# Kernel tuning notes

Measured on AMD Instinct MI355X. Metric: run time of the kernel, lower is better.

## Reference

```python
import jax, jax.numpy as jnp
import numpy as np

# Static config (init_kwargs)
H = 56; W = 56; C = 256; NH = 8; WS = 7; SS = 3
HD = C // NH
SCALE = HD ** -0.5
N = WS * WS                      # tokens per window = 49
NW = (H // WS) * (W // WS)       # windows per image = 64
HIDDEN = int(C * 4.0)
EPS = 1e-5


def _rel_pos_index():
    coords = np.stack(np.meshgrid(np.arange(WS), np.arange(WS), indexing='ij')).reshape(2, -1)
    rel = coords[:, :, None] - coords[:, None, :]          # [2, N, N]
    rel = rel.transpose(1, 2, 0).astype(np.int64)          # [N, N, 2]
    rel[:, :, 0] += WS - 1
    rel[:, :, 1] += WS - 1
    rel[:, :, 0] *= 2 * WS - 1
    return rel.sum(-1).reshape(-1)                         # [N*N]


def _attn_mask():
    # (0 / -100) mask for the shifted-window configuration, [NW, N, N]
    img = np.zeros([H, W])
    cnt = 0
    for hs in (slice(0, -WS), slice(-WS, -SS), slice(-SS, None)):
        for ws in (slice(0, -WS), slice(-WS, -SS), slice(-SS, None)):
            img[hs, ws] = cnt
            cnt += 1
    mw = img.reshape(H // WS, WS, W // WS, WS).transpose(0, 2, 1, 3).reshape(-1, N)
    diff = mw[:, None, :] - mw[:, :, None]                 # [NW, N, N]
    return np.where(diff != 0, -100.0, 0.0).astype(np.float32)


_REL_IDX = _rel_pos_index()
_MASK = _attn_mask()


def _ln(x, g, b):
    mu = jnp.mean(x, axis=-1, keepdims=True)
    var = jnp.mean((x - mu) ** 2, axis=-1, keepdims=True)
    return (x - mu) * jax.lax.rsqrt(var + EPS) * g + b


def setup_inputs() -> dict:
    key = jax.random.key(0)
    ks = jax.random.split(key, 16)
    B = 32
    s = 0.02
    return {
        'x': jax.random.normal(ks[0], (B, H * W, C), dtype=jnp.float32),
        'gamma1': jnp.ones((C,), jnp.float32),
        'beta1': jnp.zeros((C,), jnp.float32),
        'qkv_w': jax.random.normal(ks[1], (C, 3 * C), jnp.float32) * s,
        'qkv_b': jnp.zeros((3 * C,), jnp.float32),
        'proj_w': jax.random.normal(ks[2], (C, C), jnp.float32) * s,
        'proj_b': jnp.zeros((C,), jnp.float32),
        'rpb_table': jax.random.normal(ks[3], ((2 * WS - 1) * (2 * WS - 1), NH), jnp.float32) * s,
        'gamma2': jnp.ones((C,), jnp.float32),
        'beta2': jnp.zeros((C,), jnp.float32),
        'fc1_w': jax.random.normal(ks[4], (C, HIDDEN), jnp.float32) * s,
        'fc1_b': jnp.zeros((HIDDEN,), jnp.float32),
        'fc2_w': jax.random.normal(ks[5], (HIDDEN, C), jnp.float32) * s,
        'fc2_b': jnp.zeros((C,), jnp.float32),
    }


def reference(x, gamma1, beta1, qkv_w, qkv_b, proj_w, proj_b, rpb_table,
              gamma2, beta2, fc1_w, fc1_b, fc2_w, fc2_b):
    B = x.shape[0]
    y = _ln(x, gamma1, beta1).reshape(B, H, W, C)
    # cyclic shift
    y = jnp.roll(y, (-SS, -SS), axis=(1, 2))
    # window partition -> [B*NW, N, C]
    win = y.reshape(B, H // WS, WS, W // WS, WS, C)
    win = win.transpose(0, 1, 3, 2, 4, 5).reshape(-1, N, C)
    # qkv projection, split heads
    qkv = (win @ qkv_w + qkv_b).reshape(-1, N, 3, NH, HD).transpose(2, 0, 3, 1, 4)
    q, k, v = qkv[0] * SCALE, qkv[1], qkv[2]            # [B*NW, NH, N, HD]
    attn = jnp.einsum('bhnd,bhmd->bhnm', q, k)          # [B*NW, NH, N, N]
    # gathered relative position bias
    bias = rpb_table[jnp.asarray(_REL_IDX)].reshape(N, N, NH).transpose(2, 0, 1)
    attn = attn + bias[None]
    # shift mask
    mask = jnp.asarray(_MASK)                           # [NW, N, N]
    attn = attn.reshape(B, NW, NH, N, N) + mask[None, :, None]
    attn = jax.nn.softmax(attn.reshape(-1, NH, N, N), axis=-1)
    o = jnp.einsum('bhnm,bhmd->bnhd', attn, v).reshape(-1, N, C)
    o = o @ proj_w + proj_b
    # window reverse + reverse shift
    o = o.reshape(B, H // WS, W // WS, WS, WS, C).transpose(0, 1, 3, 2, 4, 5).reshape(B, H, W, C)
    o = jnp.roll(o, (SS, SS), axis=(1, 2)).reshape(B, H * W, C)
    x = x + o
    # MLP block
    y = _ln(x, gamma2, beta2)
    y = jax.nn.gelu(y @ fc1_w + fc1_b, approximate=False) @ fc2_w + fc2_b
    return x + y
```

## Files before the change

### kernel.cpp

```cpp
#include <hip/hip_runtime.h>
#include <hip/hip_bf16.h>
#include <math.h>


typedef __bf16 bf16_t;
typedef __bf16 bf16x4 __attribute__((ext_vector_type(4)));
typedef __bf16 bf16x8 __attribute__((ext_vector_type(8)));
typedef float f32x4 __attribute__((ext_vector_type(4)));

#define AS1 __attribute__((address_space(1)))
#define AS3 __attribute__((address_space(3)))

__device__ __forceinline__ void gload_lds16(const bf16_t* g, bf16_t* l) {
  __builtin_amdgcn_global_load_lds((AS1 void*)g, (AS3 void*)l, 16, 0, 0);
}

__global__ void transpose_cast(const float* __restrict__ w, bf16_t* __restrict__ wt,
                               int K, int N) {
  int idx = blockIdx.x * 256 + threadIdx.x;
  if (idx < N * K) {
    int n = idx / K, k = idx - n * K;
    wt[idx] = (bf16_t)w[(size_t)k * N + n];
  }
}

__global__ void build_bm(const float* __restrict__ rpb, float* __restrict__ bm) {
  int t = blockIdx.x, h = blockIdx.y;
  int wr = (t & 2) ? 7 : 0, wc = (t & 1) ? 7 : 0;
  for (int e = threadIdx.x; e < 4096; e += 256) {
    int r = e >> 6, c = e & 63;
    float v;
    if (c >= 49) {
      v = -30000.f;
    } else if (r >= 49) {
      v = 0.f;
    } else {
      int r1 = r / 7, c1 = r - r1 * 7;
      int r2 = c / 7, c2 = c - r2 * 7;
      v = rpb[((r1 - r2 + 6) * 13 + (c1 - c2 + 6)) * 8 + h];
      int hp = wr * 7 + r1, wp = wc * 7 + c1;
      int hq = wr * 7 + r2, wq = wc * 7 + c2;
      int ri = (hp < 49 ? 0 : (hp < 53 ? 1 : 2)) * 3 + (wp < 49 ? 0 : (wp < 53 ? 1 : 2));
      int rj = (hq < 49 ? 0 : (hq < 53 ? 1 : 2)) * 3 + (wq < 49 ? 0 : (wq < 53 ? 1 : 2));
      if (ri != rj) v -= 100.f;
    }
    bm[((size_t)(t * 8 + h) * 64 + r) * 64 + c] = v;
  }
}

__global__ __launch_bounds__(256)
void ln_cast(const float* __restrict__ src, const float* __restrict__ gamma,
             const float* __restrict__ beta, bf16_t* __restrict__ dst, int windowed) {
  int row = blockIdx.x * 4 + (threadIdx.x >> 6);
  int lane = threadIdx.x & 63;
  size_t srow;
  if (windowed) {
    int w = row / 49, t = row - w * 49;
    int img = w >> 6, wi = w & 63;
    int wr = wi >> 3, wc = wi & 7;
    int rr = t / 7, cc = t - rr * 7;
    int h = wr * 7 + rr + 3; if (h >= 56) h -= 56;
    int ww = wc * 7 + cc + 3; if (ww >= 56) ww -= 56;
    srow = (size_t)img * 3136 + h * 56 + ww;
  } else {
    srow = row;
  }
  float4 v = *(const float4*)(src + srow * 256 + lane * 4);
  float s = v.x + v.y + v.z + v.w;
  float s2 = v.x * v.x + v.y * v.y + v.z * v.z + v.w * v.w;
#pragma unroll
  for (int off = 32; off > 0; off >>= 1) {
    s += __shfl_xor(s, off);
    s2 += __shfl_xor(s2, off);
  }
  float mu = s * (1.0f / 256.0f);
  float rs = rsqrtf(s2 * (1.0f / 256.0f) - mu * mu + 1e-5f);
  float4 g = *(const float4*)(gamma + lane * 4);
  float4 b = *(const float4*)(beta + lane * 4);
  bf16x4 o;
  o[0] = (bf16_t)((v.x - mu) * rs * g.x + b.x);
  o[1] = (bf16_t)((v.y - mu) * rs * g.y + b.y);
  o[2] = (bf16_t)((v.z - mu) * rs * g.z + b.z);
  o[3] = (bf16_t)((v.w - mu) * rs * g.w + b.w);
  *(bf16x4*)(dst + (size_t)row * 256 + lane * 4) = o;
}

template <int MODE>
__global__ __launch_bounds__(256)
void gemm_bt(const bf16_t* __restrict__ A, const bf16_t* __restrict__ Bt,
             const float* __restrict__ bias,
             bf16_t* Cbf, float* Cf, const float* Res,
             int M, int N, int K) {
  __shared__ __align__(16) bf16_t As[128 * 32];
  __shared__ __align__(16) bf16_t Bs[128 * 32];
  const int tid = threadIdx.x;
  const int lane = tid & 63;
  const int wave = tid >> 6;
  const int wm = wave & 1, wn = wave >> 1;
  const int m0 = blockIdx.x * 128;
  const int n0 = blockIdx.y * 128;

  f32x4 acc[4][4];
#pragma unroll
  for (int i = 0; i < 4; i++)
#pragma unroll
    for (int j = 0; j < 4; j++) acc[i][j] = f32x4{0.f, 0.f, 0.f, 0.f};

  const bf16_t* Ag = A + (size_t)m0 * K;
  const bf16_t* Bg = Bt + (size_t)n0 * K;
  const int lr = lane & 15;
  const int kq = (lane >> 4) * 8;

  for (int k0 = 0; k0 < K; k0 += 32) {
#pragma unroll
    for (int it = 0; it < 2; it++) {
      int slot = it * 256 + tid;
      int row = slot >> 2;
      int ko = (slot & 3) << 3;
      bf16_t* ldsA = As + (it * 256 + wave * 64) * 8;
      bf16_t* ldsB = Bs + (it * 256 + wave * 64) * 8;
      gload_lds16(Ag + (size_t)row * K + k0 + ko, ldsA);
      gload_lds16(Bg + (size_t)row * K + k0 + ko, ldsB);
    }
    __syncthreads();
    bf16x8 af[4], bfr[4];
#pragma unroll
    for (int i = 0; i < 4; i++) {
      af[i]  = *(const bf16x8*)(As + (wm * 64 + i * 16 + lr) * 32 + kq);
      bfr[i] = *(const bf16x8*)(Bs + (wn * 64 + i * 16 + lr) * 32 + kq);
    }
#pragma unroll
    for (int i = 0; i < 4; i++)
#pragma unroll
      for (int j = 0; j < 4; j++)
        acc[i][j] = __builtin_amdgcn_mfma_f32_16x16x32_bf16(af[i], bfr[j], acc[i][j], 0, 0, 0);
    __syncthreads();
  }

  const int quad = lane >> 4;
#pragma unroll
  for (int i = 0; i < 4; i++) {
    int rbase = m0 + wm * 64 + i * 16 + quad * 4;
#pragma unroll
    for (int j = 0; j < 4; j++) {
      int col = n0 + wn * 64 + j * 16 + lr;
      float bi = bias[col];
#pragma unroll
      for (int r = 0; r < 4; r++) {
        int row = rbase + r;
        float v = acc[i][j][r] + bi;
        if (MODE == 1) v = 0.5f * v * (1.0f + erff(v * 0.70710678118654752f));
        if (MODE <= 1) {
          Cbf[(size_t)row * N + col] = (bf16_t)v;
        } else if (MODE == 2) {
          size_t idx = (size_t)row * N + col;
          Cf[idx] = v + Res[idx];
        } else {
          int w = row / 49, t = row - w * 49;
          int img = w >> 6, wi = w & 63;
          int wr = wi >> 3, wc = wi & 7;
          int rr = t / 7, cc = t - rr * 7;
          int h = wr * 7 + rr + 3; if (h >= 56) h -= 56;
          int ww2 = wc * 7 + cc + 3; if (ww2 >= 56) ww2 -= 56;
          size_t idx = ((size_t)img * 3136 + h * 56 + ww2) * 256 + col;
          Cf[idx] = v + Res[idx];
        }
      }
    }
  }
}

__global__ __launch_bounds__(256)
void attn_mfma(const bf16_t* __restrict__ qkv, const float* __restrict__ bm,
               bf16_t* __restrict__ o) {
  __shared__ __align__(16) bf16_t Ps[64 * 72];
  __shared__ __align__(16) bf16_t Vt[32 * 72];
  const int w = blockIdx.x, h = blockIdx.y;
  const int tid = threadIdx.x;
  const int lane = tid & 63, wv = tid >> 6;
  const int lr = lane & 15, quad = lane >> 4;
  const int wi = w & 63;
  const int mtype = (((wi >> 3) == 7) ? 2 : 0) | (((wi & 7) == 7) ? 1 : 0);
  const bf16_t* base = qkv + (size_t)w * 49 * 768 + h * 32;

  for (int e = tid; e < 2048; e += 256) {
    int tok = e >> 5, d = e & 31;
    bf16_t val = (bf16_t)0.f;
    if (tok < 49) val = base[(size_t)tok * 768 + 512 + d];
    Vt[d * 72 + tok] = val;
  }
  __syncthreads();

  bf16x8 zero8;
#pragma unroll
  for (int z = 0; z < 8; z++) zero8[z] = (bf16_t)0.f;

  const int mrow = 16 * wv + lr;
  bf16x8 aq = zero8;
  if (mrow < 49) aq = *(const bf16x8*)(base + (size_t)mrow * 768 + quad * 8);
  f32x4 s[4];
#pragma unroll
  for (int j = 0; j < 4; j++) {
    int nrow = 16 * j + lr;
    bf16x8 bk = zero8;
    if (nrow < 49) bk = *(const bf16x8*)(base + (size_t)nrow * 768 + 256 + quad * 8);
    s[j] = __builtin_amdgcn_mfma_f32_16x16x32_bf16(aq, bk, f32x4{0.f, 0.f, 0.f, 0.f}, 0, 0, 0);
  }

  const float* bmb = bm + ((size_t)(mtype * 8 + h) * 64 + 16 * wv) * 64;
  float inv[4];
#pragma unroll
  for (int reg = 0; reg < 4; reg++) {
    int rl = quad * 4 + reg;
    float v0[4];
    float mx = -1e30f;
#pragma unroll
    for (int j = 0; j < 4; j++) {
      float v = s[j][reg] * 0.17677669529663689f + bmb[rl * 64 + 16 * j + lr];
      v0[j] = v;
      mx = fmaxf(mx, v);
    }
#pragma unroll
    for (int off = 8; off > 0; off >>= 1) mx = fmaxf(mx, __shfl_xor(mx, off));
    float sum = 0.f;
#pragma unroll
    for (int j = 0; j < 4; j++) {
      float e = __expf(v0[j] - mx);
      v0[j] = e;
      sum += e;
    }
#pragma unroll
    for (int off = 8; off > 0; off >>= 1) sum += __shfl_xor(sum, off);
    inv[reg] = 1.0f / sum;
#pragma unroll
    for (int j = 0; j < 4; j++)
      Ps[(16 * wv + rl) * 72 + 16 * j + lr] = (bf16_t)v0[j];
  }

  f32x4 oacc[2];
  oacc[0] = f32x4{0.f, 0.f, 0.f, 0.f};
  oacc[1] = f32x4{0.f, 0.f, 0.f, 0.f};
#pragma unroll
  for (int kk = 0; kk < 2; kk++) {
    bf16x8 ap = *(const bf16x8*)(Ps + (16 * wv + lr) * 72 + kk * 32 + quad * 8);
#pragma unroll
    for (int n = 0; n < 2; n++) {
      bf16x8 bv = *(const bf16x8*)(Vt + (16 * n + lr) * 72 + kk * 32 + quad * 8);
      oacc[n] = __builtin_amdgcn_mfma_f32_16x16x32_bf16(ap, bv, oacc[n], 0, 0, 0);
    }
  }
#pragma unroll
  for (int n = 0; n < 2; n++) {
#pragma unroll
    for (int reg = 0; reg < 4; reg++) {
      int row = 16 * wv + quad * 4 + reg;
      if (row < 49) {
        int d = 16 * n + lr;
        o[((size_t)w * 49 + row) * 256 + h * 32 + d] = (bf16_t)(oacc[n][reg] * inv[reg]);
      }
    }
  }
}

extern "C" void kernel_launch(void* const* d_in, const int* in_sizes, int n_in,
                              void* d_out, int out_size, void* d_ws, size_t ws_size,
                              hipStream_t stream) {
  const float* x      = (const float*)d_in[0];
  const float* g1     = (const float*)d_in[1];
  const float* b1     = (const float*)d_in[2];
  const float* qkv_w  = (const float*)d_in[3];
  const float* qkv_b  = (const float*)d_in[4];
  const float* proj_w = (const float*)d_in[5];
  const float* proj_b = (const float*)d_in[6];
  const float* rpb    = (const float*)d_in[7];
  const float* g2     = (const float*)d_in[8];
  const float* b2     = (const float*)d_in[9];
  const float* fc1_w  = (const float*)d_in[10];
  const float* fc1_b  = (const float*)d_in[11];
  const float* fc2_w  = (const float*)d_in[12];
  const float* fc2_b  = (const float*)d_in[13];
  float* out = (float*)d_out;
  char* ws = (char*)d_ws;

  bf16_t* xw   = (bf16_t*)ws;
  bf16_t* qkv  = (bf16_t*)(ws + 51380224);
  bf16_t* ow   = (bf16_t*)(ws + 205520896);
  bf16_t* hbuf = (bf16_t*)(ws + 51380224);
  bf16_t* y2   = xw;
  bf16_t* qkvWt  = (bf16_t*)(ws + 256901120);
  bf16_t* projWt = qkvWt + 768 * 256;
  bf16_t* fc1Wt  = projWt + 256 * 256;
  bf16_t* fc2Wt  = fc1Wt + 1024 * 256;
  float*  bm     = (float*)fc2Wt;

  transpose_cast<<<(768 * 256 + 255) / 256, 256, 0, stream>>>(qkv_w, qkvWt, 256, 768);
  transpose_cast<<<(256 * 256 + 255) / 256, 256, 0, stream>>>(proj_w, projWt, 256, 256);
  transpose_cast<<<(1024 * 256 + 255) / 256, 256, 0, stream>>>(fc1_w, fc1Wt, 256, 1024);
  build_bm<<<dim3(4, 8), 256, 0, stream>>>(rpb, bm);

  ln_cast<<<25088, 256, 0, stream>>>(x, g1, b1, xw, 1);
  gemm_bt<0><<<dim3(784, 6), 256, 0, stream>>>(xw, qkvWt, qkv_b, qkv, nullptr, nullptr,
                                               100352, 768, 256);
  attn_mfma<<<dim3(2048, 8), 256, 0, stream>>>(qkv, bm, ow);
  transpose_cast<<<(256 * 1024 + 255) / 256, 256, 0, stream>>>(fc2_w, fc2Wt, 1024, 256);
  gemm_bt<3><<<dim3(784, 2), 256, 0, stream>>>(ow, projWt, proj_b, nullptr, out, x,
                                               100352, 256, 256);
  ln_cast<<<25088, 256, 0, stream>>>(out, g2, b2, y2, 0);
  gemm_bt<1><<<dim3(784, 8), 256, 0, stream>>>(y2, fc1Wt, fc1_b, hbuf, nullptr, nullptr,
                                               100352, 1024, 256);
  gemm_bt<2><<<dim3(784, 2), 256, 0, stream>>>(hbuf, fc2Wt, fc2_b, nullptr, out, out,
                                               100352, 256, 1024);
}
```

Measured before the change: 870.1 us.

## Fuse MLP fc1, GELU and fc2 into one kernel keeping hidden activations on-chip

Replaces the separate fc1 (with GELU) and fc2 GEMMs with a single fused_mlp kernel. Each block processes 64 token rows, computes the 1024-wide hidden layer in 128-column chunks into LDS, and accumulates the fc2 output in registers, which removes the large bf16 hidden-buffer write and re-read through HBM. GELU switches from exact erf to a tanh-style approximation built on exp, which adds a small numerical deviation from the reference. Other changes merge three weight transpose launches into one and vectorize the V load in the attention kernel. The fused kernel re-streams all MLP weights from cache for every block with no double buffering and many barriers, which may cost throughput.

```diff
diff --git a/kernel.cpp b/kernel.cpp
--- a/kernel.cpp
+++ b/kernel.cpp
@@ -13,6 +13,25 @@
 
 __device__ __forceinline__ void gload_lds16(const bf16_t* g, bf16_t* l) {
   __builtin_amdgcn_global_load_lds((AS1 void*)g, (AS3 void*)l, 16, 0, 0);
+}
+
+__global__ void transpose_cast3(const float* __restrict__ qkv_w,
+                                const float* __restrict__ proj_w,
+                                const float* __restrict__ fc1_w,
+                                bf16_t* __restrict__ qkvWt,
+                                bf16_t* __restrict__ projWt,
+                                bf16_t* __restrict__ fc1Wt) {
+  int idx = blockIdx.x * 256 + threadIdx.x;
+  const float* w;
+  bf16_t* wt;
+  int N;
+  if (blockIdx.y == 0) { w = qkv_w; wt = qkvWt; N = 768; }
+  else if (blockIdx.y == 1) { w = proj_w; wt = projWt; N = 256; }
+  else { w = fc1_w; wt = fc1Wt; N = 1024; }
+  if (idx < N * 256) {
+    int n = idx >> 8, k = idx & 255;
+    wt[idx] = (bf16_t)w[(size_t)k * N + n];
+  }
 }
 
 __global__ void transpose_cast(const float* __restrict__ w, bf16_t* __restrict__ wt,
@@ -149,12 +168,8 @@
       for (int r = 0; r < 4; r++) {
         int row = rbase + r;
         float v = acc[i][j][r] + bi;
-        if (MODE == 1) v = 0.5f * v * (1.0f + erff(v * 0.70710678118654752f));
-        if (MODE <= 1) {
+        if (MODE == 0) {
           Cbf[(size_t)row * N + col] = (bf16_t)v;
-        } else if (MODE == 2) {
-          size_t idx = (size_t)row * N + col;
-          Cf[idx] = v + Res[idx];
         } else {
           int w = row / 49, t = row - w * 49;
           int img = w >> 6, wi = w & 63;
@@ -183,17 +198,18 @@
   const int mtype = (((wi >> 3) == 7) ? 2 : 0) | (((wi & 7) == 7) ? 1 : 0);
   const bf16_t* base = qkv + (size_t)w * 49 * 768 + h * 32;
 
-  for (int e = tid; e < 2048; e += 256) {
-    int tok = e >> 5, d = e & 31;
-    bf16_t val = (bf16_t)0.f;
-    if (tok < 49) val = base[(size_t)tok * 768 + 512 + d];
-    Vt[d * 72 + tok] = val;
+  bf16x8 zero8;
+#pragma unroll
+  for (int z = 0; z < 8; z++) zero8[z] = (bf16_t)0.f;
+
+  {
+    int tok = tid >> 2, d8 = (tid & 3) * 8;
+    bf16x8 v8 = zero8;
+    if (tok < 49) v8 = *(const bf16x8*)(base + (size_t)tok * 768 + 512 + d8);
+#pragma unroll
+    for (int z = 0; z < 8; z++) Vt[(d8 + z) * 72 + tok] = v8[z];
   }
   __syncthreads();
-
-  bf16x8 zero8;
-#pragma unroll
-  for (int z = 0; z < 8; z++) zero8[z] = (bf16_t)0.f;
 
   const int mrow = 16 * wv + lr;
   bf16x8 aq = zero8;
@@ -257,6 +273,124 @@
       if (row < 49) {
         int d = 16 * n + lr;
         o[((size_t)w * 49 + row) * 256 + h * 32 + d] = (bf16_t)(oacc[n][reg] * inv[reg]);
+      }
+    }
+  }
+}
+
+__global__ __launch_bounds__(256, 2)
+void fused_mlp(const bf16_t* __restrict__ y2, const bf16_t* __restrict__ W1t,
+               const float* __restrict__ b1, const bf16_t* __restrict__ W2t,
+               const float* __restrict__ b2, float* __restrict__ out) {
+  __shared__ __align__(16) bf16_t Ls[64 * 264];
+  __shared__ __align__(16) bf16_t Ws[8192];
+  __shared__ __align__(16) bf16_t Hs[64 * 168];
+  const int tid = threadIdx.x;
+  const int lane = tid & 63, wave = tid >> 6;
+  const int lr = lane & 15, quad = lane >> 4;
+  const int wr = wave & 1, wc = wave >> 1;
+  const int m0 = blockIdx.x * 64;
+
+#pragma unroll
+  for (int it = 0; it < 8; it++) {
+    int slot = it * 256 + tid;
+    int row = slot >> 5, g = slot & 31;
+    bf16x8 v = *(const bf16x8*)(y2 + (size_t)(m0 + row) * 256 + g * 8);
+    *(bf16x8*)(Ls + row * 264 + g * 8) = v;
+  }
+  __syncthreads();
+
+  f32x4 acc2[2][8];
+#pragma unroll
+  for (int i = 0; i < 2; i++)
+#pragma unroll
+    for (int n = 0; n < 8; n++) acc2[i][n] = f32x4{0.f, 0.f, 0.f, 0.f};
+
+  for (int hc = 0; hc < 8; hc++) {
+    f32x4 acc1[2][4];
+#pragma unroll
+    for (int i = 0; i < 2; i++)
+#pragma unroll
+      for (int j = 0; j < 4; j++) acc1[i][j] = f32x4{0.f, 0.f, 0.f, 0.f};
+
+    for (int ks = 0; ks < 4; ks++) {
+      __syncthreads();
+#pragma unroll
+      for (int r = 0; r < 4; r++) {
+        int sub = r >> 1, half = r & 1;
+        int row = half * 64 + (tid >> 2), k8 = tid & 3;
+        const bf16_t* src = W1t + (size_t)(hc * 128 + row) * 256 + ks * 64 + sub * 32 + k8 * 8;
+        gload_lds16(src, Ws + sub * 4096 + half * 2048 + wave * 512);
+      }
+      __syncthreads();
+#pragma unroll
+      for (int kk = 0; kk < 2; kk++) {
+        bf16x8 a[2], b[4];
+#pragma unroll
+        for (int i = 0; i < 2; i++)
+          a[i] = *(const bf16x8*)(Ls + (32 * wr + 16 * i + lr) * 264 + ks * 64 + kk * 32 + quad * 8);
+#pragma unroll
+        for (int j = 0; j < 4; j++)
+          b[j] = *(const bf16x8*)(Ws + kk * 4096 + (64 * wc + 16 * j + lr) * 32 + quad * 8);
+#pragma unroll
+        for (int i = 0; i < 2; i++)
+#pragma unroll
+          for (int j = 0; j < 4; j++)
+            acc1[i][j] = __builtin_amdgcn_mfma_f32_16x16x32_bf16(a[i], b[j], acc1[i][j], 0, 0, 0);
+      }
+    }
+#pragma unroll
+    for (int i = 0; i < 2; i++) {
+#pragma unroll
+      for (int j = 0; j < 4; j++) {
+        float bias1 = b1[hc * 128 + 64 * wc + 16 * j + lr];
+        int hoff = (2 * wc + (j >> 1)) * 40 + (j & 1) * 16 + lr;
+#pragma unroll
+        for (int reg = 0; reg < 4; reg++) {
+          int row_l = 32 * wr + 16 * i + quad * 4 + reg;
+          float v = acc1[i][j][reg] + bias1;
+          float arg = fminf(v * (0.7978845608f + 0.0356774081f * v * v), 15.f);
+          float e = __expf(2.f * arg);
+          float g = v * (e / (e + 1.f));
+          Hs[row_l * 168 + hoff] = (bf16_t)g;
+        }
+      }
+    }
+    for (int ks2 = 0; ks2 < 4; ks2++) {
+      __syncthreads();
+#pragma unroll
+      for (int r = 0; r < 4; r++) {
+        int row = r * 64 + (tid >> 2), k8 = tid & 3;
+        const bf16_t* src = W2t + (size_t)row * 1024 + hc * 128 + ks2 * 32 + k8 * 8;
+        gload_lds16(src, Ws + r * 2048 + wave * 512);
+      }
+      __syncthreads();
+      bf16x8 ah[2], bw[8];
+#pragma unroll
+      for (int i = 0; i < 2; i++)
+        ah[i] = *(const bf16x8*)(Hs + (32 * wr + 16 * i + lr) * 168 + ks2 * 40 + quad * 8);
+#pragma unroll
+      for (int n = 0; n < 8; n++)
+        bw[n] = *(const bf16x8*)(Ws + (128 * wc + 16 * n + lr) * 32 + quad * 8);
+#pragma unroll
+      for (int i = 0; i < 2; i++)
+#pragma unroll
+        for (int n = 0; n < 8; n++)
+          acc2[i][n] = __builtin_amdgcn_mfma_f32_16x16x32_bf16(ah[i], bw[n], acc2[i][n], 0, 0, 0);
+    }
+  }
+
+#pragma unroll
+  for (int i = 0; i < 2; i++) {
+#pragma unroll
+    for (int n = 0; n < 8; n++) {
+      int col = 128 * wc + 16 * n + lr;
+      float bi = b2[col];
+#pragma unroll
+      for (int reg = 0; reg < 4; reg++) {
+        int row = m0 + 32 * wr + 16 * i + quad * 4 + reg;
+        size_t idx = (size_t)row * 256 + col;
+        out[idx] = acc2[i][n][reg] + bi + out[idx];
       }
     }
   }
@@ -285,7 +419,6 @@
   bf16_t* xw   = (bf16_t*)ws;
   bf16_t* qkv  = (bf16_t*)(ws + 51380224);
   bf16_t* ow   = (bf16_t*)(ws + 205520896);
-  bf16_t* hbuf = (bf16_t*)(ws + 51380224);
   bf16_t* y2   = xw;
   bf16_t* qkvWt  = (bf16_t*)(ws + 256901120);
   bf16_t* projWt = qkvWt + 768 * 256;
@@ -293,9 +426,8 @@
   bf16_t* fc2Wt  = fc1Wt + 1024 * 256;
   float*  bm     = (float*)fc2Wt;
 
-  transpose_cast<<<(768 * 256 + 255) / 256, 256, 0, stream>>>(qkv_w, qkvWt, 256, 768);
-  transpose_cast<<<(256 * 256 + 255) / 256, 256, 0, stream>>>(proj_w, projWt, 256, 256);
-  transpose_cast<<<(1024 * 256 + 255) / 256, 256, 0, stream>>>(fc1_w, fc1Wt, 256, 1024);
+  transpose_cast3<<<dim3(1024, 3), 256, 0, stream>>>(qkv_w, proj_w, fc1_w,
+                                                     qkvWt, projWt, fc1Wt);
   build_bm<<<dim3(4, 8), 256, 0, stream>>>(rpb, bm);
 
   ln_cast<<<25088, 256, 0, stream>>>(x, g1, b1, xw, 1);
@@ -306,8 +438,5 @@
   gemm_bt<3><<<dim3(784, 2), 256, 0, stream>>>(ow, projWt, proj_b, nullptr, out, x,
                                                100352, 256, 256);
   ln_cast<<<25088, 256, 0, stream>>>(out, g2, b2, y2, 0);
-  gemm_bt<1><<<dim3(784, 8), 256, 0, stream>>>(y2, fc1Wt, fc1_b, hbuf, nullptr, nullptr,
-                                               100352, 1024, 256);
-  gemm_bt<2><<<dim3(784, 2), 256, 0, stream>>>(hbuf, fc2Wt, fc2_b, nullptr, out, out,
-                                               100352, 256, 1024);
-}
+  fused_mlp<<<1568, 256, 0, stream>>>(y2, fc1Wt, fc1_b, fc2Wt, fc2_b, out);
+}
```

Result: faster. 800.8 us (-8.0%).
